# Performance work log

Hardware: AMD Instinct MI355X
Metric: run time of the kernel (lower is better)

Reference implementation:

```python
import jax, jax.numpy as jnp
import numpy as np
import math

B, T, E = 1, 2048, 1024
H = 8                      # num_heads
D = E // H // 2            # head_dim = 64
LAMBDA_INIT = 0.8 - 0.6 * math.exp(-0.3 * 1)  # depth=1
SCALE_BASE = 512.0
THETA = 10000.0


def _rope_tables(T, d):
    # lucidrains rotary-embedding-torch, use_xpos=True, interleaved pairs
    inv_freq = 1.0 / (THETA ** (jnp.arange(0, d, 2, dtype=jnp.float32) / d))
    pos = jnp.arange(T, dtype=jnp.float32)
    freqs = pos[:, None] * inv_freq[None, :]            # (T, d/2)
    freqs = jnp.repeat(freqs, 2, axis=-1)               # (T, d) interleaved
    sv = (jnp.arange(0, d, 2, dtype=jnp.float32) + 0.4 * d) / (1.4 * d)
    power = (pos - T // 2) / SCALE_BASE
    scale = sv[None, :] ** power[:, None]               # (T, d/2)
    scale = jnp.concatenate([scale, scale], axis=-1)    # (T, d)
    return freqs, scale


def _rotate_half(x):
    # interleaved rotate: (..., d) pairs (x1, x2) -> (-x2, x1)
    x1 = x[..., 0::2]
    x2 = x[..., 1::2]
    return jnp.stack([-x2, x1], axis=-1).reshape(x.shape)


def _apply_rope(t, freqs, scale):
    # t: (B, T, h, d); freqs/scale: (T, d) broadcast over heads
    f = freqs[None, :, None, :]
    s = scale[None, :, None, :]
    return t * jnp.cos(f) * s + _rotate_half(t) * jnp.sin(f) * s


def setup_inputs() -> dict:
    key = jax.random.key(0)
    ks = jax.random.split(key, 9)
    w = 0.02
    return {
        "x": jax.random.normal(ks[0], (B, T, E), dtype=jnp.float32),
        "Wq": jax.random.normal(ks[1], (E, E), dtype=jnp.float32) * w,
        "Wk": jax.random.normal(ks[2], (E, E), dtype=jnp.float32) * w,
        "Wv": jax.random.normal(ks[3], (E, E), dtype=jnp.float32) * w,
        "Wo": jax.random.normal(ks[4], (E, E), dtype=jnp.float32) * w,
        "lambda_q1": jax.random.normal(ks[5], (D,), dtype=jnp.float32) * 0.1,
        "lambda_k1": jax.random.normal(ks[6], (D,), dtype=jnp.float32) * 0.1,
        "lambda_q2": jax.random.normal(ks[7], (D,), dtype=jnp.float32) * 0.1,
        "lambda_k2": jax.random.normal(ks[8], (D,), dtype=jnp.float32) * 0.1,
    }


def reference(x, Wq, Wk, Wv, Wo, lambda_q1, lambda_k1, lambda_q2, lambda_k2):
    b, t, e = x.shape
    scaling = D ** -0.5

    q = (x @ Wq.T).reshape(b, t, 2 * H, D)
    k = (x @ Wk.T).reshape(b, t, 2 * H, D)   # n_rep = 1
    v = (x @ Wv.T).reshape(b, t, H, 2 * D)

    freqs, scale = _rope_tables(t, D)
    q = _apply_rope(q, freqs, scale)
    k = _apply_rope(k, freqs, 1.0 / scale)   # xpos: keys use scale**-1

    q = jnp.transpose(q, (0, 2, 1, 3)) * scaling   # (B, 2H, T, D)
    k = jnp.transpose(k, (0, 2, 1, 3))             # (B, 2H, T, D)
    v = jnp.transpose(v, (0, 2, 1, 3))             # (B, H, T, 2D)

    scores = jnp.einsum('bhtd,bhsd->bhts', q, k)
    probs = jax.nn.softmax(scores.astype(jnp.float32), axis=-1).astype(scores.dtype)

    lam1 = jnp.exp(jnp.sum(lambda_q1 * lambda_k1))
    lam2 = jnp.exp(jnp.sum(lambda_q2 * lambda_k2))
    lam = lam1 - lam2 + LAMBDA_INIT

    probs = probs.reshape(b, H, 2, t, t)
    diff = probs[:, :, 0] - lam * probs[:, :, 1]   # (B, H, T, T)

    attn = jnp.einsum('bhts,bhsd->bhtd', diff, v)  # (B, H, T, 2D)
    # RMSNorm (no affine), eps=1e-5
    attn = attn * jax.lax.rsqrt(jnp.mean(attn * attn, axis=-1, keepdims=True) + 1e-5)
    attn = attn * (1.0 - LAMBDA_INIT)

    attn = jnp.transpose(attn, (0, 2, 1, 3)).reshape(b, t, e)
    return attn @ Wo.T
```

## Files before the change

### kernel.cpp

```cpp
#include <hip/hip_runtime.h>
#include <hip/hip_bf16.h>

typedef __hip_bfloat16 bf16;
typedef _Float16 f16;
typedef __attribute__((ext_vector_type(8))) __bf16 bf16x8;
typedef __attribute__((ext_vector_type(8))) _Float16 f16x8;
typedef __attribute__((ext_vector_type(4))) _Float16 f16x4;
typedef __attribute__((ext_vector_type(4))) float floatx4;
typedef __attribute__((ext_vector_type(16))) float floatx16;

#define T_SEQ 2048
#define EMB   1024
#define LAMBDA_INIT 0.35550906759096926f

__device__ __forceinline__ bf16 f2bf(float f) {
  unsigned u;
  __builtin_memcpy(&u, &f, 4);
  u += 0x7FFF + ((u >> 16) & 1);
  unsigned short h = (unsigned short)(u >> 16);
  bf16 r;
  __builtin_memcpy(&r, &h, 2);
  return r;
}

__device__ __forceinline__ int cvtpk_bf16(float lo, float hi) {
  int r;
  asm("v_cvt_pk_bf16_f32 %0, %1, %2" : "=v"(r) : "v"(lo), "v"(hi));
  return r;
}

__device__ __forceinline__ void permswap(int& a, int& b) {
  asm volatile("v_permlane32_swap_b32 %0, %1" : "+v"(a), "+v"(b));
}

__device__ __forceinline__ void gl_lds16(const void* g, void* l) {
  __builtin_amdgcn_global_load_lds((const __attribute__((address_space(1))) void*)g,
                                   (__attribute__((address_space(3))) void*)l, 16, 0, 0);
}

__device__ __forceinline__ floatx4 mfma_h(f16x8 a, f16x8 b, floatx4 c) {
  return __builtin_amdgcn_mfma_f32_16x16x32_f16(a, b, c, 0, 0, 0);
}
__device__ __forceinline__ floatx16 mfma32_h(f16x8 a, f16x8 b, floatx16 c) {
  return __builtin_amdgcn_mfma_f32_32x32x16_f16(a, b, c, 0, 0, 0);
}
__device__ __forceinline__ floatx16 mfma32_bf(bf16x8 a, bf16x8 b, floatx16 c) {
  return __builtin_amdgcn_mfma_f32_32x32x16_bf16(a, b, c, 0, 0, 0);
}

__global__ __launch_bounds__(256) void convert_kernel(
    const float* __restrict__ x,  const float* __restrict__ wq,
    const float* __restrict__ wk, const float* __restrict__ wv,
    const float* __restrict__ wo,
    f16* __restrict__ xf, f16* __restrict__ wqf, f16* __restrict__ wkf,
    f16* __restrict__ wvf, f16* __restrict__ wof)
{
  int b = blockIdx.x;
  const float* src; f16* dst; long off;
  if      (b < 2048) { src = x;  dst = xf;  off = (long)b * 1024; }
  else if (b < 3072) { src = wq; dst = wqf; off = (long)(b - 2048) * 1024; }
  else if (b < 4096) { src = wk; dst = wkf; off = (long)(b - 3072) * 1024; }
  else if (b < 5120) { src = wv; dst = wvf; off = (long)(b - 4096) * 1024; }
  else               { src = wo; dst = wof; off = (long)(b - 5120) * 1024; }
  long i = off + threadIdx.x * 4;
  float4 v = *(const float4*)(src + i);
  f16x4 o;
  o.x = (f16)v.x; o.y = (f16)v.y; o.z = (f16)v.z; o.w = (f16)v.w;
  *(f16x4*)(dst + i) = o;
}

template <int MODE>
__device__ __forceinline__ void gemm64x128_f16(
    const f16* __restrict__ A_, const f16* __restrict__ B_,
    void* C0v, int Kld, int Klen, int ldc, int m0, int n0, char* smem)
{
  const int tid  = threadIdx.x;
  const int wave = tid >> 6, lane = tid & 63, quad = lane >> 4, l16 = lane & 15;
  const int mo = (wave & 1) << 5;
  const int no = (wave >> 1) << 6;

  floatx4 acc[2][4];
  #pragma unroll
  for (int i = 0; i < 2; i++)
    #pragma unroll
    for (int j = 0; j < 4; j++) { acc[i][j][0]=0.f; acc[i][j][1]=0.f; acc[i][j][2]=0.f; acc[i][j][3]=0.f; }

  const int srow = tid >> 3;
  const int ch   = (tid & 7) ^ (srow & 7);
  const long aoff = (long)(m0 + srow) * Kld + ch * 8;
  const long boff = (long)(n0 + srow) * Kld + ch * 8;
  const int wb = wave << 10;

  #pragma unroll
  for (int rr = 0; rr < 2; rr++)
    gl_lds16(A_ + aoff + (long)rr * 32 * Kld, smem + wb + rr * 4096);
  #pragma unroll
  for (int rr = 0; rr < 4; rr++)
    gl_lds16(B_ + boff + (long)rr * 32 * Kld, smem + 8192 + wb + rr * 4096);

  for (int k0 = 0; k0 < Klen; k0 += 64) {
    const int cur = (k0 >> 6) & 1;
    const char* sb = smem + cur * 24576;

    asm volatile("s_waitcnt vmcnt(0)" ::: "memory");
    asm volatile("s_barrier" ::: "memory");

    const f16* As = (const f16*)sb;
    const f16* Bs = (const f16*)(sb + 8192);

    f16x8 a[2][2], b[2][4];
    #pragma unroll
    for (int kt = 0; kt < 2; kt++) {
      #pragma unroll
      for (int i = 0; i < 2; i++) {
        int m = mo + i * 16 + l16;
        a[kt][i] = *(const f16x8*)(As + m * 64 + ((((kt << 2) | quad) ^ (m & 7)) << 3));
      }
      #pragma unroll
      for (int j = 0; j < 4; j++) {
        int n = no + j * 16 + l16;
        b[kt][j] = *(const f16x8*)(Bs + n * 64 + ((((kt << 2) | quad) ^ (n & 7)) << 3));
      }
    }

    if (k0 + 64 < Klen) {
      char* nb = smem + (cur ^ 1) * 24576;
      #pragma unroll
      for (int rr = 0; rr < 2; rr++)
        gl_lds16(A_ + aoff + k0 + 64 + (long)rr * 32 * Kld, nb + wb + rr * 4096);
      #pragma unroll
      for (int rr = 0; rr < 4; rr++)
        gl_lds16(B_ + boff + k0 + 64 + (long)rr * 32 * Kld, nb + 8192 + wb + rr * 4096);
    }

    #pragma unroll
    for (int kt = 0; kt < 2; kt++)
      #pragma unroll
      for (int i = 0; i < 2; i++)
        #pragma unroll
        for (int j = 0; j < 4; j++)
          acc[i][j] = mfma_h(a[kt][i], b[kt][j], acc[i][j]);
  }
  __syncthreads();

  if (MODE == 1) {
    #pragma unroll
    for (int i = 0; i < 2; i++)
      #pragma unroll
      for (int j = 0; j < 4; j++)
        #pragma unroll
        for (int r = 0; r < 4; r++) {
          int row = m0 + mo + i * 16 + quad * 4 + r;
          int col = n0 + no + j * 16 + l16;
          ((float*)C0v)[(long)row * ldc + col] = acc[i][j][r];
        }
  } else {
    unsigned short* E = (unsigned short*)smem;
    #pragma unroll
    for (int i = 0; i < 2; i++)
      #pragma unroll
      for (int j = 0; j < 4; j++)
        #pragma unroll
        for (int r = 0; r < 4; r++) {
          int row = mo + i * 16 + quad * 4 + r;
          int col = no + j * 16 + l16;
          float v = acc[i][j][r];
          unsigned short bits;
          if (MODE == 0) {
            bf16 t = f2bf(v);
            __builtin_memcpy(&bits, &t, 2);
          } else {
            float p = __shfl_xor(v, 1, 64);
            int d = col & 63;
            float fr = (float)(m0 + row) * __expf((float)(d >> 1) * -0.28782313662425574f);
            float sn, cs;
            sincosf(fr, &sn, &cs);
            float rot = (col & 1) ? fmaf(v, cs, p * sn) : fmaf(v, cs, -p * sn);
            float power = (float)(m0 + row - 1024) * (1.0f / 512.0f);
            if (MODE == 3) power = -power;
            float sv = fmaf(2.0f, (float)(d & 31), 25.6f) * (1.0f / 89.6f);
            float s = __expf(power * __logf(sv));
            float ov = rot * s;
            if (MODE == 2) ov *= 0.125f;
            f16 t = (f16)ov;
            __builtin_memcpy(&bits, &t, 2);
          }
          E[row * 128 + col] = bits;
        }
    __syncthreads();
    const int rr0 = tid >> 4;
    const int c8  = (tid & 15) * 8;
    #pragma unroll
    for (int p2 = 0; p2 < 4; p2++) {
      int row = p2 * 16 + rr0;
      *(uint4*)((unsigned short*)C0v + (long)(m0 + row) * ldc + n0 + c8) =
          *(const uint4*)(E + row * 128 + c8);
    }
  }
}

__global__ __launch_bounds__(256) void qkv_gemm(
    const f16* __restrict__ xf,
    const f16* __restrict__ wqf, const f16* __restrict__ wkf,
    const f16* __restrict__ wvf,
    f16* __restrict__ qf, f16* __restrict__ kf, bf16* __restrict__ vt)
{
  __shared__ char smem[49152];
  int bid = blockIdx.x;
  if (bid < 256) {
    gemm64x128_f16<2>(xf, wqf, qf, 1024, 1024, 1024, (bid >> 3) * 64, (bid & 7) * 128, smem);
  } else if (bid < 512) {
    bid -= 256;
    gemm64x128_f16<3>(xf, wkf, kf, 1024, 1024, 1024, (bid >> 3) * 64, (bid & 7) * 128, smem);
  } else {
    bid -= 512;
    gemm64x128_f16<0>(wvf, xf, vt, 1024, 1024, 2048, (bid >> 4) * 64, (bid & 15) * 128, smem);
  }
}

__global__ __launch_bounds__(256) void out_gemm(const f16* __restrict__ attn,
                                                const f16* __restrict__ Wo,
                                                float* __restrict__ p0,
                                                float* __restrict__ p1)
{
  __shared__ char smem[49152];
  int bid = blockIdx.x;
  const int kh = bid >> 8;
  const int b  = bid & 255;
  float* pb = kh ? p1 : p0;
  gemm64x128_f16<1>(attn + kh * 512, Wo + kh * 512, pb, 1024, 512, 1024,
                    (b >> 3) * 64, (b & 7) * 128, smem);
}

__global__ __launch_bounds__(256) void add_out(const float* __restrict__ p0,
                                               const float* __restrict__ p1,
                                               float* __restrict__ out)
{
  long i = ((long)blockIdx.x * 256 + threadIdx.x) * 4;
  float4 a = *(const float4*)(p0 + i);
  float4 b = *(const float4*)(p1 + i);
  float4 c;
  c.x = a.x + b.x; c.y = a.y + b.y; c.z = a.z + b.z; c.w = a.w + b.w;
  *(float4*)(out + i) = c;
}

__global__ __launch_bounds__(256) void diff_attn(
    const f16* __restrict__ qf_, const f16* __restrict__ kf_,
    const bf16* __restrict__ vt,
    const float* __restrict__ lq1, const float* __restrict__ lk1,
    const float* __restrict__ lq2, const float* __restrict__ lk2,
    f16* __restrict__ attn)
{
  __shared__ char smem[65536];
  const int tid  = threadIdx.x;
  const int wave = tid >> 6, lane = tid & 63;
  const int l32 = lane & 31, lh = lane >> 5;
  const int h  = blockIdx.x & 7;
  const int qb = blockIdx.x >> 3;
  const int hl = wave >> 1;
  const int ws = wave & 1;
  const int hh = h * 2 + hl;
  const int t0 = qb * 32;

  float a1 = lq1[lane] * lk1[lane];
  float a2 = lq2[lane] * lk2[lane];
  #pragma unroll
  for (int off = 1; off < 64; off <<= 1) {
    a1 += __shfl_xor(a1, off, 64);
    a2 += __shfl_xor(a2, off, 64);
  }
  const float lam = __expf(a1) - __expf(a2) + LAMBDA_INIT;

  f16x8 qfr[4];
  {
    const f16* qrow = qf_ + (long)(t0 + l32) * EMB + hh * 64 + lh * 8;
    #pragma unroll
    for (int kt = 0; kt < 4; kt++) qfr[kt] = *(const f16x8*)(qrow + kt * 16);
  }

  floatx16 o[4];
  #pragma unroll
  for (int nt = 0; nt < 4; nt++)
    #pragma unroll
    for (int r = 0; r < 16; r++) o[nt][r] = 0.f;
  float lr0 = 0.f, lr1 = 0.f, lr2 = 0.f, lr3 = 0.f;

  const int srow = lane >> 3;
  const int ch   = (lane & 7) ^ srow;
  const f16*  kgp = kf_ + (long)(h * 2 + ws) * 64 + (long)srow * EMB + ch * 8;
  const bf16* vgp = vt + (long)(h * 128 + (wave - 2) * 64 + srow) * T_SEQ + ch * 8;
  const int kofs = wave * 8192;
  const int vofs = 16384 + (wave - 2) * 8192;

  if (wave < 2) {
    #pragma unroll
    for (int j = 0; j < 8; j++)
      gl_lds16(kgp + (long)j * 8 * EMB, smem + kofs + j * 1024);
  } else {
    #pragma unroll
    for (int j = 0; j < 8; j++)
      gl_lds16(vgp + (long)j * 8 * T_SEQ, smem + vofs + j * 1024);
  }

  for (int kb = 0; kb < T_SEQ; kb += 64) {
    const int cur = (kb >> 6) & 1;
    const char* sb = smem + cur * 32768;

    asm volatile("s_waitcnt vmcnt(0)" ::: "memory");
    asm volatile("s_barrier" ::: "memory");

    const f16*  Ks  = (const f16*)(sb + hl * 8192);
    const bf16* Vsb = (const bf16*)(sb + 16384);

    f16x8 kfr[4];
    #pragma unroll
    for (int kt = 0; kt < 4; kt++) {
      int krow = ws * 32 + l32;
      int c = kt * 2 + lh;
      kfr[kt] = *(const f16x8*)(Ks + krow * 64 + ((c ^ (krow & 7)) << 3));
    }
    bf16x8 vfr[4][2];
    #pragma unroll
    for (int nt = 0; nt < 4; nt++) {
      #pragma unroll
      for (int kt = 0; kt < 2; kt++) {
        int vrow = nt * 32 + l32;
        int c = ws * 4 + kt * 2 + lh;
        vfr[nt][kt] = *(const bf16x8*)(Vsb + vrow * 64 + ((c ^ (vrow & 7)) << 3));
      }
    }

    if (kb + 64 < T_SEQ) {
      char* nb = smem + (cur ^ 1) * 32768;
      if (wave < 2) {
        #pragma unroll
        for (int j = 0; j < 8; j++)
          gl_lds16(kgp + (long)(kb + 64) * EMB + (long)j * 8 * EMB,
                   nb + kofs + j * 1024);
      } else {
        #pragma unroll
        for (int j = 0; j < 8; j++)
          gl_lds16(vgp + (kb + 64) + (long)j * 8 * T_SEQ,
                   nb + vofs + j * 1024);
      }
    }

    floatx16 s;
    #pragma unroll
    for (int r = 0; r < 16; r++) s[r] = 0.f;
    #pragma unroll
    for (int kt = 0; kt < 4; kt++)
      s = mfma32_h(kfr[kt], qfr[kt], s);
    #pragma unroll
    for (int r = 0; r < 4; r++) {
      float p0 = __builtin_amdgcn_exp2f(
          fmaf(s[r], 1.4426950408889634f, -17.312340490667562f));
      float p1 = __builtin_amdgcn_exp2f(
          fmaf(s[r + 4], 1.4426950408889634f, -17.312340490667562f));
      float p2 = __builtin_amdgcn_exp2f(
          fmaf(s[r + 8], 1.4426950408889634f, -17.312340490667562f));
      float p3 = __builtin_amdgcn_exp2f(
          fmaf(s[r + 12], 1.4426950408889634f, -17.312340490667562f));
      s[r] = p0; s[r + 4] = p1; s[r + 8] = p2; s[r + 12] = p3;
      lr0 += p0; lr1 += p1; lr2 += p2; lr3 += p3;
    }
    bf16x8 pf[2];
    #pragma unroll
    for (int kt = 0; kt < 2; kt++) {
      const int b0 = kt * 8;
      int w0 = cvtpk_bf16(s[b0 + 0], s[b0 + 1]);
      int w1 = cvtpk_bf16(s[b0 + 2], s[b0 + 3]);
      int w2 = cvtpk_bf16(s[b0 + 4], s[b0 + 5]);
      int w3 = cvtpk_bf16(s[b0 + 6], s[b0 + 7]);
      permswap(w0, w2);
      permswap(w1, w3);
      union { int i[4]; bf16x8 v; } u;
      u.i[0] = w0; u.i[1] = w1; u.i[2] = w2; u.i[3] = w3;
      pf[kt] = u.v;
    }
    #pragma unroll
    for (int nt = 0; nt < 4; nt++) {
      #pragma unroll
      for (int kt = 0; kt < 2; kt++)
        o[nt] = mfma32_bf(pf[kt], vfr[nt][kt], o[nt]);
    }
  }
  __syncthreads();

  float lr = (lr0 + lr1) + (lr2 + lr3);
  float lrw = lr + __shfl_xor(lr, 32, 64);

  float* Cb = (float*)smem;
  float* Lb = (float*)(smem + 32768);

  if (ws == 1) {
    #pragma unroll
    for (int r = 0; r < 16; r++) {
      int m = (r & 3) + 8 * (r >> 2) + 4 * lh;
      #pragma unroll
      for (int nt = 0; nt < 4; nt++)
        Cb[hl * 4096 + m * 128 + nt * 32 + l32] = o[nt][r];
    }
  }
  if (lh == 0) Lb[ws * 64 + hl * 32 + l32] = lrw;
  __syncthreads();
  if (ws == 0) {
    #pragma unroll
    for (int r = 0; r < 16; r++) {
      int m = (r & 3) + 8 * (r >> 2) + 4 * lh;
      float inv = 1.0f / (Lb[hl * 32 + m] + Lb[64 + hl * 32 + m]);
      #pragma unroll
      for (int nt = 0; nt < 4; nt++)
        o[nt][r] = (o[nt][r] + Cb[hl * 4096 + m * 128 + nt * 32 + l32]) * inv;
    }
  }
  __syncthreads();
  if (hl == 1 && ws == 0) {
    #pragma unroll
    for (int r = 0; r < 16; r++) {
      int m = (r & 3) + 8 * (r >> 2) + 4 * lh;
      #pragma unroll
      for (int nt = 0; nt < 4; nt++)
        Cb[4096 + m * 128 + nt * 32 + l32] = o[nt][r];
    }
  }
  __syncthreads();
  if (hl == 0 && ws == 0) {
    float ss[16];
    #pragma unroll
    for (int r = 0; r < 16; r++) {
      int m = (r & 3) + 8 * (r >> 2) + 4 * lh;
      ss[r] = 0.f;
      #pragma unroll
      for (int nt = 0; nt < 4; nt++) {
        float v = o[nt][r] - lam * Cb[4096 + m * 128 + nt * 32 + l32];
        o[nt][r] = v;
        ss[r] += v * v;
      }
    }
    #pragma unroll
    for (int r = 0; r < 16; r++) {
      ss[r] += __shfl_xor(ss[r], 1, 64);
      ss[r] += __shfl_xor(ss[r], 2, 64);
      ss[r] += __shfl_xor(ss[r], 4, 64);
      ss[r] += __shfl_xor(ss[r], 8, 64);
      ss[r] += __shfl_xor(ss[r], 16, 64);
      float rms = rsqrtf(ss[r] * (1.0f / 128.0f) + 1e-5f) * (1.0f - LAMBDA_INIT);
      int m = (r & 3) + 8 * (r >> 2) + 4 * lh;
      #pragma unroll
      for (int nt = 0; nt < 4; nt++)
        attn[(long)(t0 + m) * EMB + h * 128 + nt * 32 + l32] = (f16)(o[nt][r] * rms);
    }
  }
}

extern "C" void kernel_launch(void* const* d_in, const int* in_sizes, int n_in,
                              void* d_out, int out_size, void* d_ws, size_t ws_size,
                              hipStream_t stream)
{
  (void)in_sizes; (void)n_in; (void)out_size; (void)ws_size;
  const float* x   = (const float*)d_in[0];
  const float* Wq  = (const float*)d_in[1];
  const float* Wk  = (const float*)d_in[2];
  const float* Wv  = (const float*)d_in[3];
  const float* Wo  = (const float*)d_in[4];
  const float* lq1 = (const float*)d_in[5];
  const float* lk1 = (const float*)d_in[6];
  const float* lq2 = (const float*)d_in[7];
  const float* lk2 = (const float*)d_in[8];
  float* out = (float*)d_out;

  const size_t TM = (size_t)T_SEQ * EMB;
  const size_t WM = (size_t)EMB * EMB;
  bf16* vtws = (bf16*)d_ws;
  f16*  aws  = (f16*)(vtws + TM);
  f16*  xf   = aws  + TM;
  f16*  wqf  = xf   + TM;
  f16*  wkf  = wqf  + WM;
  f16*  wvf  = wkf  + WM;
  f16*  wof  = wvf  + WM;
  f16*  qf   = wof  + WM;
  f16*  kf   = qf   + TM;

  float* p0 = (float*)xf;
  float* p1 = (float*)qf;

  convert_kernel<<<6144, 256, 0, stream>>>(x, Wq, Wk, Wv, Wo,
                                           xf, wqf, wkf, wvf, wof);
  qkv_gemm<<<768, 256, 0, stream>>>(xf, wqf, wkf, wvf, qf, kf, vtws);
  diff_attn<<<512, 256, 0, stream>>>(qf, kf, vtws, lq1, lk1, lq2, lk2, aws);
  out_gemm<<<512, 256, 0, stream>>>(aws, wof, p0, p1);
  add_out<<<2048, 256, 0, stream>>>(p0, p1, out);
}
```

Baseline: 191.1 us.

## Load QKV GEMM operands directly from global memory into MFMA registers

Adds a GEMM variant for the QKV projection that skips LDS staging of the A and B tiles. Each wave loads its MFMA fragments straight from global memory, and the LDS allocation shrinks to what the epilogue needs. The aim is to remove LDS write/read traffic and barriers and to raise occupancy. The cost is redundant, less coalesced global loads, since operands are reused across waves only through cache, with no explicit double buffering.

```diff
diff --git a/kernel.cpp b/kernel.cpp
--- a/kernel.cpp
+++ b/kernel.cpp
@@ -70,6 +70,90 @@
 }
 
 template <int MODE>
+__device__ __forceinline__ void gemm64x128_direct(
+    const f16* __restrict__ A_, const f16* __restrict__ B_,
+    void* C0v, int Kld, int Klen, int ldc, int m0, int n0, char* smem)
+{
+  const int tid  = threadIdx.x;
+  const int wave = tid >> 6, lane = tid & 63, quad = lane >> 4, l16 = lane & 15;
+  const int mo = (wave & 1) << 5;
+  const int no = (wave >> 1) << 6;
+
+  floatx4 acc[2][4];
+  #pragma unroll
+  for (int i = 0; i < 2; i++)
+    #pragma unroll
+    for (int j = 0; j < 4; j++) { acc[i][j][0]=0.f; acc[i][j][1]=0.f; acc[i][j][2]=0.f; acc[i][j][3]=0.f; }
+
+  const f16* a0p = A_ + (long)(m0 + mo + l16) * Kld + quad * 8;
+  const f16* a1p = a0p + (long)16 * Kld;
+  const f16* b0p = B_ + (long)(n0 + no + l16) * Kld + quad * 8;
+  const f16* b1p = b0p + (long)16 * Kld;
+  const f16* b2p = b0p + (long)32 * Kld;
+  const f16* b3p = b0p + (long)48 * Kld;
+
+  #pragma unroll 4
+  for (int k0 = 0; k0 < Klen; k0 += 32) {
+    f16x8 a0 = *(const f16x8*)(a0p + k0);
+    f16x8 a1 = *(const f16x8*)(a1p + k0);
+    f16x8 b0 = *(const f16x8*)(b0p + k0);
+    f16x8 b1 = *(const f16x8*)(b1p + k0);
+    f16x8 b2 = *(const f16x8*)(b2p + k0);
+    f16x8 b3 = *(const f16x8*)(b3p + k0);
+    acc[0][0] = mfma_h(a0, b0, acc[0][0]);
+    acc[0][1] = mfma_h(a0, b1, acc[0][1]);
+    acc[0][2] = mfma_h(a0, b2, acc[0][2]);
+    acc[0][3] = mfma_h(a0, b3, acc[0][3]);
+    acc[1][0] = mfma_h(a1, b0, acc[1][0]);
+    acc[1][1] = mfma_h(a1, b1, acc[1][1]);
+    acc[1][2] = mfma_h(a1, b2, acc[1][2]);
+    acc[1][3] = mfma_h(a1, b3, acc[1][3]);
+  }
+
+  unsigned short* E = (unsigned short*)smem;
+  #pragma unroll
+  for (int i = 0; i < 2; i++)
+    #pragma unroll
+    for (int j = 0; j < 4; j++)
+      #pragma unroll
+      for (int r = 0; r < 4; r++) {
+        int row = mo + i * 16 + quad * 4 + r;
+        int col = no + j * 16 + l16;
+        float v = acc[i][j][r];
+        unsigned short bits;
+        if (MODE == 0) {
+          bf16 t = f2bf(v);
+          __builtin_memcpy(&bits, &t, 2);
+        } else {
+          float p = __shfl_xor(v, 1, 64);
+          int d = col & 63;
+          float fr = (float)(m0 + row) * __expf((float)(d >> 1) * -0.28782313662425574f);
+          float sn, cs;
+          sincosf(fr, &sn, &cs);
+          float rot = (col & 1) ? fmaf(v, cs, p * sn) : fmaf(v, cs, -p * sn);
+          float power = (float)(m0 + row - 1024) * (1.0f / 512.0f);
+          if (MODE == 3) power = -power;
+          float sv = fmaf(2.0f, (float)(d & 31), 25.6f) * (1.0f / 89.6f);
+          float s = __expf(power * __logf(sv));
+          float ov = rot * s;
+          if (MODE == 2) ov *= 0.125f;
+          f16 t = (f16)ov;
+          __builtin_memcpy(&bits, &t, 2);
+        }
+        E[row * 128 + col] = bits;
+      }
+  __syncthreads();
+  const int rr0 = tid >> 4;
+  const int c8  = (tid & 15) * 8;
+  #pragma unroll
+  for (int p2 = 0; p2 < 4; p2++) {
+    int row = p2 * 16 + rr0;
+    *(uint4*)((unsigned short*)C0v + (long)(m0 + row) * ldc + n0 + c8) =
+        *(const uint4*)(E + row * 128 + c8);
+  }
+}
+
+template <int MODE>
 __device__ __forceinline__ void gemm64x128_f16(
     const f16* __restrict__ A_, const f16* __restrict__ B_,
     void* C0v, int Kld, int Klen, int ldc, int m0, int n0, char* smem)
@@ -154,48 +238,6 @@
           int col = n0 + no + j * 16 + l16;
           ((float*)C0v)[(long)row * ldc + col] = acc[i][j][r];
         }
-  } else {
-    unsigned short* E = (unsigned short*)smem;
-    #pragma unroll
-    for (int i = 0; i < 2; i++)
-      #pragma unroll
-      for (int j = 0; j < 4; j++)
-        #pragma unroll
-        for (int r = 0; r < 4; r++) {
-          int row = mo + i * 16 + quad * 4 + r;
-          int col = no + j * 16 + l16;
-          float v = acc[i][j][r];
-          unsigned short bits;
-          if (MODE == 0) {
-            bf16 t = f2bf(v);
-            __builtin_memcpy(&bits, &t, 2);
-          } else {
-            float p = __shfl_xor(v, 1, 64);
-            int d = col & 63;
-            float fr = (float)(m0 + row) * __expf((float)(d >> 1) * -0.28782313662425574f);
-            float sn, cs;
-            sincosf(fr, &sn, &cs);
-            float rot = (col & 1) ? fmaf(v, cs, p * sn) : fmaf(v, cs, -p * sn);
-            float power = (float)(m0 + row - 1024) * (1.0f / 512.0f);
-            if (MODE == 3) power = -power;
-            float sv = fmaf(2.0f, (float)(d & 31), 25.6f) * (1.0f / 89.6f);
-            float s = __expf(power * __logf(sv));
-            float ov = rot * s;
-            if (MODE == 2) ov *= 0.125f;
-            f16 t = (f16)ov;
-            __builtin_memcpy(&bits, &t, 2);
-          }
-          E[row * 128 + col] = bits;
-        }
-    __syncthreads();
-    const int rr0 = tid >> 4;
-    const int c8  = (tid & 15) * 8;
-    #pragma unroll
-    for (int p2 = 0; p2 < 4; p2++) {
-      int row = p2 * 16 + rr0;
-      *(uint4*)((unsigned short*)C0v + (long)(m0 + row) * ldc + n0 + c8) =
-          *(const uint4*)(E + row * 128 + c8);
-    }
   }
 }
 
@@ -205,16 +247,16 @@
     const f16* __restrict__ wvf,
     f16* __restrict__ qf, f16* __restrict__ kf, bf16* __restrict__ vt)
 {
-  __shared__ char smem[49152];
+  __shared__ char smem[16384];
   int bid = blockIdx.x;
   if (bid < 256) {
-    gemm64x128_f16<2>(xf, wqf, qf, 1024, 1024, 1024, (bid >> 3) * 64, (bid & 7) * 128, smem);
+    gemm64x128_direct<2>(xf, wqf, qf, 1024, 1024, 1024, (bid >> 3) * 64, (bid & 7) * 128, smem);
   } else if (bid < 512) {
     bid -= 256;
-    gemm64x128_f16<3>(xf, wkf, kf, 1024, 1024, 1024, (bid >> 3) * 64, (bid & 7) * 128, smem);
+    gemm64x128_direct<3>(xf, wkf, kf, 1024, 1024, 1024, (bid >> 3) * 64, (bid & 7) * 128, smem);
   } else {
     bid -= 512;
-    gemm64x128_f16<0>(wvf, xf, vt, 1024, 1024, 2048, (bid >> 4) * 64, (bid & 15) * 128, smem);
+    gemm64x128_direct<0>(wvf, xf, vt, 1024, 1024, 2048, (bid >> 4) * 64, (bid & 15) * 128, smem);
   }
 }
 
```

Result: slower. 205.4 us (+7.5%).
